# Optimization experiments

Measured on AMD Instinct MI355X. Metric: run time of the kernel, lower is better.

Reference implementation:

```python
import jax, jax.numpy as jnp
import numpy as np
from jax import lax

DN = ('NCHW', 'OIHW', 'NCHW')

def conv7(x, w, b):
    y = lax.conv_general_dilated(x, w, window_strides=(1, 1), padding='VALID', dimension_numbers=DN)
    return y + b[None, :, None, None]

def maxpool2(x):
    return lax.reduce_window(x, -jnp.inf, lax.max, (1, 1, 2, 2), (1, 1, 2, 2), 'VALID')

def setup_inputs() -> dict:
    key = jax.random.key(0)
    ks = jax.random.split(key, 7)
    B, C, H, W = 8, 64, 70, 70
    x = jax.random.normal(ks[0], (B, C, H, W), dtype=jnp.float32)
    s = 0.05  # small init to keep softmax logits sane
    theta_w = jax.random.normal(ks[1], (100, C, 7, 7), dtype=jnp.float32) * s
    theta_b = jax.random.normal(ks[2], (100,), dtype=jnp.float32) * s
    phi_w = jax.random.normal(ks[3], (100, C, 7, 7), dtype=jnp.float32) * s
    phi_b = jax.random.normal(ks[4], (100,), dtype=jnp.float32) * s
    g_w = jax.random.normal(ks[5], (200, C, 7, 7), dtype=jnp.float32) * s
    g_b = jax.random.normal(ks[6], (200,), dtype=jnp.float32) * s
    return {'x': x, 'theta_w': theta_w, 'theta_b': theta_b, 'phi_w': phi_w, 'phi_b': phi_b, 'g_w': g_w, 'g_b': g_b}

def reference(x, theta_w, theta_b, phi_w, phi_b, g_w, g_b):
    B, C, H, W = x.shape
    h, w = H - 6, W - 6           # VALID 7x7 conv output spatial
    N = h * w                     # 4096
    M = N // 4                    # 1024 (after 2x2 maxpool)
    theta = conv7(x, theta_w, theta_b).reshape(B, 100, N)
    phi = maxpool2(conv7(x, phi_w, phi_b)).reshape(B, 100, M)
    attn = jnp.einsum('bcn,bcm->bnm', theta, phi)                # B x N x M
    attn = jax.nn.softmax(attn, axis=-1)
    g = maxpool2(conv7(x, g_w, g_b)).reshape(B, 200, M)
    attn_g = jnp.einsum('bcm,bnm->bcn', g, attn)
    return attn_g.reshape(B, 200, h, w)
```

## Files before the change

### kernel.cpp

```cpp
#include <hip/hip_runtime.h>
#include <cstdint>
#include <cstddef>

#define BATCH 8
#define CIN 64
#define HIN 70
#define HOUT 64
#define NPIX 4096
#define MPIX 1024

typedef __attribute__((ext_vector_type(8))) short short8;
typedef __attribute__((ext_vector_type(4))) float f32x4;
typedef __attribute__((ext_vector_type(4))) unsigned int uint4v;

__device__ __forceinline__ unsigned short f2bf_rne(float f) {
  unsigned int u = __builtin_bit_cast(unsigned int, f);
  unsigned int r = (u + 0x7FFFu + ((u >> 16) & 1u)) >> 16;
  return (unsigned short)r;
}

__device__ __forceinline__ unsigned int rot16(unsigned int u) {
  return (u >> 16) | (u << 16);
}

__global__ __launch_bounds__(256) void prep_x(const float* __restrict__ x,
                                              unsigned int* __restrict__ xTi) {
  __shared__ float tile[64][71];
  const int blk = blockIdx.x;
  const int b = blk / 70;
  const int r = blk - b * 70;
  const int t = threadIdx.x;
  for (int i = t; i < 64 * 70; i += 256) {
    int ci = i / 70;
    int c = i - ci * 70;
    tile[ci][c] = x[(((size_t)(b * 64 + ci)) * 70 + r) * 70 + c];
  }
  __syncthreads();
  for (int i = t; i < 70 * 64; i += 256) {
    int c = i >> 6;
    int ci = i & 63;
    float a = tile[ci][c];
    unsigned short hi = f2bf_rne(a);
    float hif = __builtin_bit_cast(float, ((unsigned int)hi) << 16);
    unsigned short lo = f2bf_rne(a - hif);
    xTi[(((size_t)(b * 70 + r)) * 70 + c) * 64 + ci] =
        (unsigned int)hi | (((unsigned int)lo) << 16);
  }
}

__global__ __launch_bounds__(256) void prep_w(
    const float* __restrict__ tw, const float* __restrict__ pw,
    const float* __restrict__ gw,
    const float* __restrict__ tb, const float* __restrict__ pb,
    const float* __restrict__ gb,
    unsigned int* __restrict__ wTi, float* __restrict__ biasPad) {
  int gid = blockIdx.x * 256 + threadIdx.x;
  if (gid >= 49 * 448 * 64) return;
  if (gid < 448) {
    float bv = 0.0f;
    if (gid < 100) bv = tb[gid];
    else if (gid < 200) bv = pb[gid - 100];
    else if (gid < 400) bv = gb[gid - 200];
    biasPad[gid] = bv;
  }
  int ci = gid & 63;
  int OC = (gid >> 6) % 448;
  int s = gid / (448 * 64);
  float v = 0.0f;
  if (OC < 100) v = tw[((size_t)(OC * 64 + ci)) * 49 + s];
  else if (OC < 200) v = pw[((size_t)((OC - 100) * 64 + ci)) * 49 + s];
  else if (OC < 400) v = gw[((size_t)((OC - 200) * 64 + ci)) * 49 + s];
  unsigned short hi = f2bf_rne(v);
  float hif = __builtin_bit_cast(float, ((unsigned int)hi) << 16);
  unsigned short lo = f2bf_rne(v - hif);
  wTi[gid] = (unsigned int)hi | (((unsigned int)lo) << 16);
}

__global__ __launch_bounds__(512, 2) void convmfma_kernel(
    const unsigned short* __restrict__ xTi,
    const unsigned short* __restrict__ wTi,
    const float* __restrict__ biasPad,
    unsigned int* __restrict__ thd_dw,
    unsigned int* __restrict__ phd_dw,
    unsigned short* __restrict__ gP) {
  __shared__ __align__(16) char smem[62720 + 16384];
  const int LDSW = 62720;

  const int gx = blockIdx.x;
  const int b = gx >> 3;
  const int ptile = gx & 7;
  const int oy0 = ptile * 8;
  const int oc0 = blockIdx.y << 6;

  const int t = threadIdx.x;
  const int wv = t >> 6;
  const int l = t & 63;
  const int lm = l & 15;
  const int lg = l >> 4;
  const int py = oy0 + wv;

  const int sub = t >> 8;
  const int oc_t = (t >> 2) & 63;
  const int q = t & 3;
  const int wdstOff =
      sub * 4096 + (oc_t << 6) + ((q << 4) ^ (((oc_t >> 1) & 3) << 4));
  const int keyA = ((lm >> 1) & 3) << 4;
  const int laneA = (lm << 6) + ((lg << 4) ^ keyA);

  f32x4 acc[4][4];
#pragma unroll
  for (int j = 0; j < 4; ++j)
#pragma unroll
    for (int f = 0; f < 4; ++f) acc[j][f] = (f32x4)0.0f;

  for (int chunk = 0; chunk < 4; ++chunk) {
    for (int i = t; i < 3920; i += 512) {
      int idx70 = i >> 2;
      int s16 = i & 3;
      int rr = idx70 / 70;
      int cc = idx70 - rr * 70;
      const unsigned short* src =
          xTi + ((((size_t)(b * 70 + oy0 + rr)) * 70 + cc) << 7) +
          (chunk << 5) + (s16 << 3);
      short8 v = *(const short8*)src;
      int dst = (idx70 << 6) + ((s16 << 4) ^ (((cc >> 1) & 3) << 4));
      *(short8*)(smem + dst) = v;
    }
    const unsigned short* wsrcBase =
        wTi + ((size_t)(oc0 + oc_t) << 7) + (chunk << 5) + (q << 3);
    short8 wreg = *(const short8*)(wsrcBase + (size_t)sub * 57344);
    *(short8*)(smem + LDSW + wdstOff) = wreg;
    wreg = *(const short8*)(wsrcBase + (size_t)(2 + sub) * 57344);
    __syncthreads();

    for (int p = 0; p < 25; ++p) {
      const char* slotBase = smem + LDSW + ((p & 1) << 13);
#pragma unroll
      for (int halfs = 0; halfs < 2; ++halfs) {
        const int s = 2 * p + halfs;
        if (s <= 48) {
          const int ky = s / 7;
          const int kx = s - ky * 7;
          const char* wb = slotBase + (halfs << 12) + laneA;
          short8 aW[4], aS[4];
#pragma unroll
          for (int j = 0; j < 4; ++j) {
            aW[j] = *(const short8*)(wb + j * 1024);
            uint4v u = __builtin_bit_cast(uint4v, aW[j]);
            u.x = rot16(u.x); u.y = rot16(u.y);
            u.z = rot16(u.z); u.w = rot16(u.w);
            aS[j] = __builtin_bit_cast(short8, u);
          }
          const int klx = kx + lm;
          const int key = ((klx >> 1) & 3) << 4;
          const char* bbase =
              smem + ((wv + ky) * 70 + klx) * 64 + ((lg << 4) ^ key);
#pragma unroll
          for (int f = 0; f < 4; ++f) {
            short8 bf = *(const short8*)(bbase + f * 1024);
#pragma unroll
            for (int j = 0; j < 4; ++j) {
              acc[j][f] = __builtin_amdgcn_mfma_f32_16x16x32_bf16(
                  aW[j], bf, acc[j][f], 0, 0, 0);
              acc[j][f] = __builtin_amdgcn_mfma_f32_16x16x32_bf16(
                  aS[j], bf, acc[j][f], 0, 0, 0);
            }
          }
        }
      }
      if (p < 24) {
        *(short8*)(smem + LDSW + (((p + 1) & 1) << 13) + wdstOff) = wreg;
        if (p < 23) {
          int snext = 2 * (p + 2) + sub;
          if (snext > 48) snext = 48;
          wreg = *(const short8*)(wsrcBase + (size_t)snext * 57344);
        }
      }
      __syncthreads();
    }
  }

  float bia[4][4];
#pragma unroll
  for (int j = 0; j < 4; ++j)
#pragma unroll
    for (int r = 0; r < 4; ++r) bia[j][r] = biasPad[oc0 + j * 16 + lg * 4 + r];

#pragma unroll
  for (int j = 0; j < 4; ++j) {
#pragma unroll
    for (int f = 0; f < 4; ++f) {
#pragma unroll
      for (int r = 0; r < 4; ++r) {
        int ch = oc0 + j * 16 + lg * 4 + r;
        int n = py * 64 + f * 16 + lm;
        if (ch < 100) {
          float v = acc[j][f][r] + bia[j][r];
          unsigned short hi = f2bf_rne(v);
          float hif = __builtin_bit_cast(float, ((unsigned int)hi) << 16);
          unsigned short lo = f2bf_rne(v - hif);
          thd_dw[(((size_t)(b << 12) + n) << 7) + ch] =
              (unsigned int)hi | (((unsigned int)lo) << 16);
        } else if (ch < 128) {
          thd_dw[(((size_t)(b << 12) + n) << 7) + ch] = 0u;
        }
      }
    }
  }

  __syncthreads();
  float* scratch = (float*)smem;

#pragma unroll
  for (int j = 0; j < 4; ++j) {
#pragma unroll
    for (int f = 0; f < 4; ++f) {
#pragma unroll
      for (int r = 0; r < 4; ++r) {
        float v = acc[j][f][r] + bia[j][r];
        float vn = fmaxf(v, __shfl_xor(v, 1));
        acc[j][f][r] = vn;
        if ((wv & 1) && !(lm & 1)) {
          int ch_local = j * 16 + lg * 4 + r;
          int mcol = f * 8 + (lm >> 1);
          scratch[(wv >> 1) * 2112 + ch_local * 33 + mcol] = vn;
        }
      }
    }
  }
  __syncthreads();

  if (!(wv & 1)) {
#pragma unroll
    for (int j = 0; j < 4; ++j) {
#pragma unroll
      for (int f = 0; f < 4; ++f) {
#pragma unroll
        for (int r = 0; r < 4; ++r) {
          if (!(lm & 1)) {
            int ch = oc0 + j * 16 + lg * 4 + r;
            int ch_local = j * 16 + lg * 4 + r;
            int mcol = f * 8 + (lm >> 1);
            float partner = scratch[(wv >> 1) * 2112 + ch_local * 33 + mcol];
            float vfinal = fmaxf(acc[j][f][r], partner);
            int m = (((oy0 >> 1) + (wv >> 1)) << 5) + mcol;
            if (ch >= 100 && ch < 200) {
              int c = ch - 100;
              unsigned short hi = f2bf_rne(vfinal);
              float hif = __builtin_bit_cast(float, ((unsigned int)hi) << 16);
              unsigned short lo = f2bf_rne(vfinal - hif);
              phd_dw[(((size_t)(b << 10) + m) << 7) + c] =
                  (unsigned int)hi | (((unsigned int)lo) << 16);
            } else if (ch >= 200 && ch < 408) {
              int cg = ch - 200;
              gP[((size_t)(b * 208 + cg) << 10) + m] = f2bf_rne(vfinal);
              if (ch < 228) {
                phd_dw[(((size_t)(b << 10) + m) << 7) + (ch - 100)] = 0u;
              }
            }
          }
        }
      }
    }
  }
}

__global__ __launch_bounds__(256) void attn_kernel(
    const unsigned short* __restrict__ thd,
    const unsigned short* __restrict__ phd,
    const unsigned short* __restrict__ gP,
    float* __restrict__ out) {
  __shared__ __align__(16) float outAcc[16][212];
  __shared__ float corrL[16][33];
  __shared__ float statsL[4][16][2];
  __shared__ float mFinL[16];
  __shared__ float invL[16];

  const int bx = blockIdx.x;
  const int b = bx >> 8;
  const int n0 = (bx & 255) << 4;
  const int t = threadIdx.x;
  const int w = t >> 6;
  const int l = t & 63;
  const int lm = l & 15;
  const int lg = l >> 4;

  short8 aA[8], aS[8];
  {
    const unsigned short* ap =
        thd + (((size_t)(b << 12) + n0 + lm) << 8) + lg * 8;
#pragma unroll
    for (int kf = 0; kf < 8; ++kf) {
      short8 v = *(const short8*)(ap + kf * 32);
      aA[kf] = v;
      uint4v u = __builtin_bit_cast(uint4v, v);
      u.x = rot16(u.x); u.y = rot16(u.y); u.z = rot16(u.z); u.w = rot16(u.w);
      aS[kf] = __builtin_bit_cast(short8, u);
    }
  }

  float mRun = -3.0e38f, sRun = 0.0f;
  unsigned int Pr[8][4];

  const int src1 = ((lg & 1) << 5) + lm;
  const int src2 = src1 + 16;
  const bool hi2 = (lg >> 1) != 0;

#pragma unroll
  for (int step = 0; step < 8; ++step) {
    const int m0 = (w << 8) + (step << 5);
    f32x4 ac0 = (f32x4)0.f, ac1 = (f32x4)0.f;
    const unsigned short* bp0 =
        phd + (((size_t)(b << 10) + m0 + lm) << 8) + lg * 8;
    const unsigned short* bp1 = bp0 + (16 << 8);
#pragma unroll
    for (int kf = 0; kf < 8; ++kf) {
      short8 av0 = *(const short8*)(bp0 + kf * 32);
      short8 av1 = *(const short8*)(bp1 + kf * 32);
      ac0 = __builtin_amdgcn_mfma_f32_16x16x32_bf16(av0, aA[kf], ac0, 0, 0, 0);
      ac1 = __builtin_amdgcn_mfma_f32_16x16x32_bf16(av1, aA[kf], ac1, 0, 0, 0);
      ac0 = __builtin_amdgcn_mfma_f32_16x16x32_bf16(av0, aS[kf], ac0, 0, 0, 0);
      ac1 = __builtin_amdgcn_mfma_f32_16x16x32_bf16(av1, aS[kf], ac1, 0, 0, 0);
    }
    float tm = fmaxf(fmaxf(fmaxf(ac0[0], ac0[1]), fmaxf(ac0[2], ac0[3])),
                     fmaxf(fmaxf(ac1[0], ac1[1]), fmaxf(ac1[2], ac1[3])));
    tm = fmaxf(tm, __shfl_xor(tm, 16));
    tm = fmaxf(tm, __shfl_xor(tm, 32));
    float mNew = fmaxf(mRun, tm);
    float scale = __expf(mRun - mNew);
    float p0 = __expf(ac0[0] - mNew), p1 = __expf(ac0[1] - mNew);
    float p2 = __expf(ac0[2] - mNew), p3 = __expf(ac0[3] - mNew);
    float q0 = __expf(ac1[0] - mNew), q1 = __expf(ac1[1] - mNew);
    float q2 = __expf(ac1[2] - mNew), q3 = __expf(ac1[3] - mNew);
    float cs = ((p0 + p1) + (p2 + p3)) + ((q0 + q1) + (q2 + q3));
    cs += __shfl_xor(cs, 16);
    cs += __shfl_xor(cs, 32);
    mRun = mNew;
    sRun = sRun * scale + cs;
    if (l < 16) corrL[lm][(w << 3) + step] = mRun;
    unsigned int d0 = (unsigned int)f2bf_rne(p0) |
                      (((unsigned int)f2bf_rne(p1)) << 16);
    unsigned int d1 = (unsigned int)f2bf_rne(p2) |
                      (((unsigned int)f2bf_rne(p3)) << 16);
    unsigned int e0 = (unsigned int)f2bf_rne(q0) |
                      (((unsigned int)f2bf_rne(q1)) << 16);
    unsigned int e1 = (unsigned int)f2bf_rne(q2) |
                      (((unsigned int)f2bf_rne(q3)) << 16);
    unsigned int A0 = (unsigned int)__shfl((int)d0, src1);
    unsigned int A1 = (unsigned int)__shfl((int)d1, src1);
    unsigned int B0 = (unsigned int)__shfl((int)d0, src2);
    unsigned int B1 = (unsigned int)__shfl((int)d1, src2);
    unsigned int C0 = (unsigned int)__shfl((int)e0, src1);
    unsigned int C1 = (unsigned int)__shfl((int)e1, src1);
    unsigned int D0 = (unsigned int)__shfl((int)e0, src2);
    unsigned int D1 = (unsigned int)__shfl((int)e1, src2);
    Pr[step][0] = hi2 ? C0 : A0;
    Pr[step][1] = hi2 ? C1 : A1;
    Pr[step][2] = hi2 ? D0 : B0;
    Pr[step][3] = hi2 ? D1 : B1;
  }
  if (l < 16) {
    statsL[w][lm][0] = mRun;
    statsL[w][lm][1] = sRun;
  }
  __syncthreads();

  if (t < 16) {
    float mF = -3.0e38f;
#pragma unroll
    for (int qq = 0; qq < 4; ++qq) mF = fmaxf(mF, statsL[qq][t][0]);
    float sF = 0.0f;
#pragma unroll
    for (int qq = 0; qq < 4; ++qq)
      sF += statsL[qq][t][1] * __expf(statsL[qq][t][0] - mF);
    mFinL[t] = mF;
    invL[t] = 1.0f / sF;
  }
  __syncthreads();

  {
    int e = t * 2;
#pragma unroll
    for (int i = 0; i < 2; ++i) {
      int row = (e + i) >> 5;
      int col = (e + i) & 31;
      corrL[row][col] = __expf(corrL[row][col] - mFinL[row]) * invL[row];
    }
  }
  __syncthreads();

#pragma unroll
  for (int s = 0; s < 8; ++s) {
    float corr = corrL[lm][(w << 3) + s];
#pragma unroll
    for (int j = 0; j < 4; ++j) {
      unsigned int u = Pr[s][j];
      float lo = __builtin_bit_cast(float, u << 16);
      float hi = __builtin_bit_cast(float, u & 0xffff0000u);
      Pr[s][j] = (unsigned int)f2bf_rne(lo * corr) |
                 (((unsigned int)f2bf_rne(hi * corr)) << 16);
    }
  }

  f32x4 oacc[13];
#pragma unroll
  for (int i = 0; i < 13; ++i) oacc[i] = (f32x4)0.f;

#pragma unroll
  for (int s = 0; s < 8; ++s) {
    uint4v pu;
    pu.x = Pr[s][0]; pu.y = Pr[s][1]; pu.z = Pr[s][2]; pu.w = Pr[s][3];
    short8 pf = __builtin_bit_cast(short8, pu);
    const unsigned short* gbase =
        gP + ((size_t)(b * 208) << 10) + (w << 8) + (s << 5) + lg * 8;
#pragma unroll
    for (int ct = 0; ct < 13; ++ct) {
      int c = (ct << 4) + lm;
      short8 gv = *(const short8*)(gbase + ((size_t)c << 10));
      oacc[ct] = __builtin_amdgcn_mfma_f32_16x16x32_bf16(pf, gv, oacc[ct], 0, 0, 0);
    }
  }

  for (int rnd = 0; rnd < 4; ++rnd) {
    if (w == rnd) {
#pragma unroll
      for (int ct = 0; ct < 13; ++ct) {
#pragma unroll
        for (int r = 0; r < 4; ++r) {
          int n = (lg << 2) + r;
          int c = (ct << 4) + lm;
          if (rnd == 0) outAcc[n][c] = oacc[ct][r];
          else outAcc[n][c] += oacc[ct][r];
        }
      }
    }
    __syncthreads();
  }

  {
    int lane16 = t & 15;
    int grp = t >> 4;
    for (int c = grp; c < 200; c += 16)
      out[(((size_t)(b * 200 + c)) << 12) + n0 + lane16] = outAcc[lane16][c];
  }
}

extern "C" void kernel_launch(void* const* d_in, const int* in_sizes, int n_in,
                              void* d_out, int out_size, void* d_ws,
                              size_t ws_size, hipStream_t stream) {
  const float* x  = (const float*)d_in[0];
  const float* tw = (const float*)d_in[1];
  const float* tb = (const float*)d_in[2];
  const float* pw = (const float*)d_in[3];
  const float* pb = (const float*)d_in[4];
  const float* gw = (const float*)d_in[5];
  const float* gb = (const float*)d_in[6];
  float* out = (float*)d_out;

  unsigned short* ws_us = (unsigned short*)d_ws;
  unsigned short* thd = ws_us;
  unsigned short* phd = ws_us + 8388608;
  unsigned short* gP  = ws_us + 10485760;
  unsigned short* xTi = ws_us + 12189696;
  unsigned short* wTi = ws_us + 17207296;
  float* biasPad = (float*)(ws_us + 20017152);

  prep_x<<<560, 256, 0, stream>>>(x, (unsigned int*)xTi);
  prep_w<<<5488, 256, 0, stream>>>(tw, pw, gw, tb, pb, gb,
                                   (unsigned int*)wTi, biasPad);

  convmfma_kernel<<<dim3(64, 7), 512, 0, stream>>>(
      xTi, wTi, biasPad, (unsigned int*)thd, (unsigned int*)phd, gP);
  attn_kernel<<<2048, 256, 0, stream>>>(thd, phd, gP, out);
}
```

Before: 502.6 us.

## Split conv into dual-bf16 theta/phi pass and single-bf16 g pass

The conv kernel is split into two template instantiations. Channels 0-255 (theta, phi and part of g) keep the hi/lo split-bf16 path with two MFMAs per product. Channels 256-447, which are only g outputs, use plain bf16 inputs with a single MFMA and half the input channels to stage, so less matrix work is spent on g. Blocks now use 256 threads, each wave computing two output rows, which lets the 2x2 maxpool happen mostly in registers instead of through LDS scratch. The price is reduced precision on part of g, extra prep buffers, and an extra launch.

Result: faster. 445.1 us (-11.4%).

```diff
diff --git a/kernel.cpp b/kernel.cpp
--- a/kernel.cpp
+++ b/kernel.cpp
@@ -24,7 +24,8 @@
 }
 
 __global__ __launch_bounds__(256) void prep_x(const float* __restrict__ x,
-                                              unsigned int* __restrict__ xTi) {
+                                              unsigned int* __restrict__ xTi,
+                                              unsigned int* __restrict__ xTi_h) {
   __shared__ float tile[64][71];
   const int blk = blockIdx.x;
   const int b = blk / 70;
@@ -46,6 +47,13 @@
     xTi[(((size_t)(b * 70 + r)) * 70 + c) * 64 + ci] =
         (unsigned int)hi | (((unsigned int)lo) << 16);
   }
+  for (int i = t; i < 70 * 32; i += 256) {
+    int c = i >> 5;
+    int dwi = i & 31;
+    unsigned int h0 = f2bf_rne(tile[2 * dwi][c]);
+    unsigned int h1 = f2bf_rne(tile[2 * dwi + 1][c]);
+    xTi_h[(((size_t)(b * 70 + r)) * 70 + c) * 32 + dwi] = h0 | (h1 << 16);
+  }
 }
 
 __global__ __launch_bounds__(256) void prep_w(
@@ -53,84 +61,112 @@
     const float* __restrict__ gw,
     const float* __restrict__ tb, const float* __restrict__ pb,
     const float* __restrict__ gb,
-    unsigned int* __restrict__ wTi, float* __restrict__ biasPad) {
+    unsigned int* __restrict__ wTi, unsigned int* __restrict__ wTi_s,
+    float* __restrict__ biasPad) {
   int gid = blockIdx.x * 256 + threadIdx.x;
-  if (gid >= 49 * 448 * 64) return;
-  if (gid < 448) {
-    float bv = 0.0f;
-    if (gid < 100) bv = tb[gid];
-    else if (gid < 200) bv = pb[gid - 100];
-    else if (gid < 400) bv = gb[gid - 200];
-    biasPad[gid] = bv;
-  }
-  int ci = gid & 63;
-  int OC = (gid >> 6) % 448;
-  int s = gid / (448 * 64);
-  float v = 0.0f;
-  if (OC < 100) v = tw[((size_t)(OC * 64 + ci)) * 49 + s];
-  else if (OC < 200) v = pw[((size_t)((OC - 100) * 64 + ci)) * 49 + s];
-  else if (OC < 400) v = gw[((size_t)((OC - 200) * 64 + ci)) * 49 + s];
-  unsigned short hi = f2bf_rne(v);
-  float hif = __builtin_bit_cast(float, ((unsigned int)hi) << 16);
-  unsigned short lo = f2bf_rne(v - hif);
-  wTi[gid] = (unsigned int)hi | (((unsigned int)lo) << 16);
-}
-
-__global__ __launch_bounds__(512, 2) void convmfma_kernel(
-    const unsigned short* __restrict__ xTi,
-    const unsigned short* __restrict__ wTi,
+  if (gid < 1404928) {
+    if (gid < 448) {
+      float bv = 0.0f;
+      if (gid < 100) bv = tb[gid];
+      else if (gid < 200) bv = pb[gid - 100];
+      else if (gid < 400) bv = gb[gid - 200];
+      biasPad[gid] = bv;
+    }
+    int ci = gid & 63;
+    int OC = (gid >> 6) % 448;
+    int s = gid / (448 * 64);
+    float v = 0.0f;
+    if (OC < 100) v = tw[((size_t)(OC * 64 + ci)) * 49 + s];
+    else if (OC < 200) v = pw[((size_t)((OC - 100) * 64 + ci)) * 49 + s];
+    else if (OC < 400) v = gw[((size_t)((OC - 200) * 64 + ci)) * 49 + s];
+    unsigned short hi = f2bf_rne(v);
+    float hif = __builtin_bit_cast(float, ((unsigned int)hi) << 16);
+    unsigned short lo = f2bf_rne(v - hif);
+    wTi[gid] = (unsigned int)hi | (((unsigned int)lo) << 16);
+  } else if (gid < 1404928 + 301056) {
+    int g2 = gid - 1404928;
+    int dwi = g2 & 31;
+    int OCl = (g2 >> 5) % 192;
+    int s = g2 / (192 * 32);
+    int gc = 56 + OCl;
+    float v0 = 0.0f, v1 = 0.0f;
+    if (gc < 200) {
+      v0 = gw[((size_t)(gc * 64 + 2 * dwi)) * 49 + s];
+      v1 = gw[((size_t)(gc * 64 + 2 * dwi + 1)) * 49 + s];
+    }
+    wTi_s[g2] = (unsigned int)f2bf_rne(v0) |
+                (((unsigned int)f2bf_rne(v1)) << 16);
+  }
+}
+
+template <bool DUAL>
+__global__ __launch_bounds__(256, 2) void convmfma_kernel(
+    const unsigned short* __restrict__ xT,
+    const unsigned short* __restrict__ wT,
     const float* __restrict__ biasPad,
     unsigned int* __restrict__ thd_dw,
     unsigned int* __restrict__ phd_dw,
     unsigned short* __restrict__ gP) {
   __shared__ __align__(16) char smem[62720 + 16384];
   const int LDSW = 62720;
+  const int NCH = DUAL ? 4 : 2;
+  const int XS = DUAL ? 128 : 64;
+  const int WOCS = DUAL ? 128 : 64;
+  const int WSTRIDE = DUAL ? 57344 : 12288;
 
   const int gx = blockIdx.x;
   const int b = gx >> 3;
   const int ptile = gx & 7;
   const int oy0 = ptile * 8;
-  const int oc0 = blockIdx.y << 6;
+  const int oc0 = (DUAL ? 0 : 256) + (blockIdx.y << 6);
+  const int oc0W = DUAL ? oc0 : (blockIdx.y << 6);
 
   const int t = threadIdx.x;
   const int wv = t >> 6;
   const int l = t & 63;
   const int lm = l & 15;
   const int lg = l >> 4;
-  const int py = oy0 + wv;
-
-  const int sub = t >> 8;
-  const int oc_t = (t >> 2) & 63;
-  const int q = t & 3;
-  const int wdstOff =
-      sub * 4096 + (oc_t << 6) + ((q << 4) ^ (((oc_t >> 1) & 3) << 4));
+
+  int wdstOff_[2];
+  const unsigned short* wsrc_[2];
   const int keyA = ((lm >> 1) & 3) << 4;
   const int laneA = (lm << 6) + ((lg << 4) ^ keyA);
 
-  f32x4 acc[4][4];
+  f32x4 acc[4][2][4];
 #pragma unroll
   for (int j = 0; j < 4; ++j)
 #pragma unroll
-    for (int f = 0; f < 4; ++f) acc[j][f] = (f32x4)0.0f;
-
-  for (int chunk = 0; chunk < 4; ++chunk) {
-    for (int i = t; i < 3920; i += 512) {
+    for (int rr = 0; rr < 2; ++rr)
+#pragma unroll
+      for (int f = 0; f < 4; ++f) acc[j][rr][f] = (f32x4)0.0f;
+
+  for (int chunk = 0; chunk < NCH; ++chunk) {
+    for (int i = t; i < 3920; i += 256) {
       int idx70 = i >> 2;
       int s16 = i & 3;
       int rr = idx70 / 70;
       int cc = idx70 - rr * 70;
       const unsigned short* src =
-          xTi + ((((size_t)(b * 70 + oy0 + rr)) * 70 + cc) << 7) +
+          xT + ((size_t)((b * 70 + oy0 + rr) * 70 + cc)) * XS +
           (chunk << 5) + (s16 << 3);
       short8 v = *(const short8*)src;
       int dst = (idx70 << 6) + ((s16 << 4) ^ (((cc >> 1) & 3) << 4));
       *(short8*)(smem + dst) = v;
     }
-    const unsigned short* wsrcBase =
-        wTi + ((size_t)(oc0 + oc_t) << 7) + (chunk << 5) + (q << 3);
-    short8 wreg = *(const short8*)(wsrcBase + (size_t)sub * 57344);
-    *(short8*)(smem + LDSW + wdstOff) = wreg;
-    wreg = *(const short8*)(wsrcBase + (size_t)(2 + sub) * 57344);
+    short8 wreg[2];
+#pragma unroll
+    for (int u2 = 0; u2 < 2; ++u2) {
+      int u = t + (u2 << 8);
+      int sub = u >> 8;
+      int oc_t = (u >> 2) & 63;
+      int q = u & 3;
+      wdstOff_[u2] =
+          sub * 4096 + (oc_t << 6) + ((q << 4) ^ (((oc_t >> 1) & 3) << 4));
+      wsrc_[u2] = wT + (size_t)(oc0W + oc_t) * WOCS + (chunk << 5) + (q << 3);
+      wreg[u2] = *(const short8*)(wsrc_[u2] + (size_t)sub * WSTRIDE);
+      *(short8*)(smem + LDSW + wdstOff_[u2]) = wreg[u2];
+      wreg[u2] = *(const short8*)(wsrc_[u2] + (size_t)(2 + sub) * WSTRIDE);
+    }
     __syncthreads();
 
     for (int p = 0; p < 25; ++p) {
@@ -146,34 +182,45 @@
 #pragma unroll
           for (int j = 0; j < 4; ++j) {
             aW[j] = *(const short8*)(wb + j * 1024);
-            uint4v u = __builtin_bit_cast(uint4v, aW[j]);
-            u.x = rot16(u.x); u.y = rot16(u.y);
-            u.z = rot16(u.z); u.w = rot16(u.w);
-            aS[j] = __builtin_bit_cast(short8, u);
+            if (DUAL) {
+              uint4v u = __builtin_bit_cast(uint4v, aW[j]);
+              u.x = rot16(u.x); u.y = rot16(u.y);
+              u.z = rot16(u.z); u.w = rot16(u.w);
+              aS[j] = __builtin_bit_cast(short8, u);
+            }
           }
           const int klx = kx + lm;
           const int key = ((klx >> 1) & 3) << 4;
-          const char* bbase =
-              smem + ((wv + ky) * 70 + klx) * 64 + ((lg << 4) ^ key);
-#pragma unroll
-          for (int f = 0; f < 4; ++f) {
-            short8 bf = *(const short8*)(bbase + f * 1024);
-#pragma unroll
-            for (int j = 0; j < 4; ++j) {
-              acc[j][f] = __builtin_amdgcn_mfma_f32_16x16x32_bf16(
-                  aW[j], bf, acc[j][f], 0, 0, 0);
-              acc[j][f] = __builtin_amdgcn_mfma_f32_16x16x32_bf16(
-                  aS[j], bf, acc[j][f], 0, 0, 0);
+#pragma unroll
+          for (int rr = 0; rr < 2; ++rr) {
+            const char* bbase =
+                smem + ((2 * wv + rr + ky) * 70 + klx) * 64 + ((lg << 4) ^ key);
+#pragma unroll
+            for (int f = 0; f < 4; ++f) {
+              short8 bf = *(const short8*)(bbase + f * 1024);
+#pragma unroll
+              for (int j = 0; j < 4; ++j) {
+                acc[j][rr][f] = __builtin_amdgcn_mfma_f32_16x16x32_bf16(
+                    aW[j], bf, acc[j][rr][f], 0, 0, 0);
+                if (DUAL)
+                  acc[j][rr][f] = __builtin_amdgcn_mfma_f32_16x16x32_bf16(
+                      aS[j], bf, acc[j][rr][f], 0, 0, 0);
+              }
             }
           }
         }
       }
       if (p < 24) {
-        *(short8*)(smem + LDSW + (((p + 1) & 1) << 13) + wdstOff) = wreg;
-        if (p < 23) {
-          int snext = 2 * (p + 2) + sub;
-          if (snext > 48) snext = 48;
-          wreg = *(const short8*)(wsrcBase + (size_t)snext * 57344);
+#pragma unroll
+        for (int u2 = 0; u2 < 2; ++u2) {
+          *(short8*)(smem + LDSW + (((p + 1) & 1) << 13) + wdstOff_[u2]) =
+              wreg[u2];
+          if (p < 23) {
+            int sub = (t + (u2 << 8)) >> 8;
+            int snext = 2 * (p + 2) + sub;
+            if (snext > 48) snext = 48;
+            wreg[u2] = *(const short8*)(wsrc_[u2] + (size_t)snext * WSTRIDE);
+          }
         }
       }
       __syncthreads();
@@ -186,78 +233,65 @@
 #pragma unroll
     for (int r = 0; r < 4; ++r) bia[j][r] = biasPad[oc0 + j * 16 + lg * 4 + r];
 
-#pragma unroll
-  for (int j = 0; j < 4; ++j) {
-#pragma unroll
-    for (int f = 0; f < 4; ++f) {
-#pragma unroll
-      for (int r = 0; r < 4; ++r) {
-        int ch = oc0 + j * 16 + lg * 4 + r;
-        int n = py * 64 + f * 16 + lm;
-        if (ch < 100) {
-          float v = acc[j][f][r] + bia[j][r];
-          unsigned short hi = f2bf_rne(v);
-          float hif = __builtin_bit_cast(float, ((unsigned int)hi) << 16);
-          unsigned short lo = f2bf_rne(v - hif);
-          thd_dw[(((size_t)(b << 12) + n) << 7) + ch] =
-              (unsigned int)hi | (((unsigned int)lo) << 16);
-        } else if (ch < 128) {
-          thd_dw[(((size_t)(b << 12) + n) << 7) + ch] = 0u;
+  if (DUAL) {
+#pragma unroll
+    for (int j = 0; j < 4; ++j) {
+#pragma unroll
+      for (int rr = 0; rr < 2; ++rr) {
+#pragma unroll
+        for (int f = 0; f < 4; ++f) {
+#pragma unroll
+          for (int r = 0; r < 4; ++r) {
+            int ch = oc0 + j * 16 + lg * 4 + r;
+            if (ch < 128) {
+              int n = (oy0 + 2 * wv + rr) * 64 + f * 16 + lm;
+              unsigned int outw = 0u;
+              if (ch < 100) {
+                float v = acc[j][rr][f][r] + bia[j][r];
+                unsigned short hi = f2bf_rne(v);
+                float hif =
+                    __builtin_bit_cast(float, ((unsigned int)hi) << 16);
+                unsigned short lo = f2bf_rne(v - hif);
+                outw = (unsigned int)hi | (((unsigned int)lo) << 16);
+              }
+              thd_dw[(((size_t)(b << 12) + n) << 7) + ch] = outw;
+            }
+          }
         }
       }
     }
   }
 
-  __syncthreads();
-  float* scratch = (float*)smem;
-
 #pragma unroll
   for (int j = 0; j < 4; ++j) {
 #pragma unroll
     for (int f = 0; f < 4; ++f) {
 #pragma unroll
       for (int r = 0; r < 4; ++r) {
-        float v = acc[j][f][r] + bia[j][r];
-        float vn = fmaxf(v, __shfl_xor(v, 1));
-        acc[j][f][r] = vn;
-        if ((wv & 1) && !(lm & 1)) {
-          int ch_local = j * 16 + lg * 4 + r;
-          int mcol = f * 8 + (lm >> 1);
-          scratch[(wv >> 1) * 2112 + ch_local * 33 + mcol] = vn;
-        }
-      }
-    }
-  }
-  __syncthreads();
-
-  if (!(wv & 1)) {
-#pragma unroll
-    for (int j = 0; j < 4; ++j) {
-#pragma unroll
-      for (int f = 0; f < 4; ++f) {
-#pragma unroll
-        for (int r = 0; r < 4; ++r) {
-          if (!(lm & 1)) {
-            int ch = oc0 + j * 16 + lg * 4 + r;
-            int ch_local = j * 16 + lg * 4 + r;
-            int mcol = f * 8 + (lm >> 1);
-            float partner = scratch[(wv >> 1) * 2112 + ch_local * 33 + mcol];
-            float vfinal = fmaxf(acc[j][f][r], partner);
-            int m = (((oy0 >> 1) + (wv >> 1)) << 5) + mcol;
+        float v0 = acc[j][0][f][r] + bia[j][r];
+        float v1 = acc[j][1][f][r] + bia[j][r];
+        float vr = fmaxf(v0, v1);
+        float vn = fmaxf(vr, __shfl_xor(vr, 1));
+        if (!(lm & 1)) {
+          int ch = oc0 + j * 16 + lg * 4 + r;
+          int m = (((oy0 >> 1) + wv) << 5) + f * 8 + (lm >> 1);
+          if (DUAL) {
             if (ch >= 100 && ch < 200) {
               int c = ch - 100;
-              unsigned short hi = f2bf_rne(vfinal);
+              unsigned short hi = f2bf_rne(vn);
               float hif = __builtin_bit_cast(float, ((unsigned int)hi) << 16);
-              unsigned short lo = f2bf_rne(vfinal - hif);
+              unsigned short lo = f2bf_rne(vn - hif);
               phd_dw[(((size_t)(b << 10) + m) << 7) + c] =
                   (unsigned int)hi | (((unsigned int)lo) << 16);
-            } else if (ch >= 200 && ch < 408) {
-              int cg = ch - 200;
-              gP[((size_t)(b * 208 + cg) << 10) + m] = f2bf_rne(vfinal);
-              if (ch < 228) {
+            } else if (ch >= 200) {
+              gP[((size_t)(b * 208 + (ch - 200)) << 10) + m] = f2bf_rne(vn);
+              if (ch < 228)
                 phd_dw[(((size_t)(b << 10) + m) << 7) + (ch - 100)] = 0u;
-              }
             }
+          } else {
+            int cg = ch - 200;
+            if (cg < 208)
+              gP[((size_t)(b * 208 + cg) << 10) + m] = f2bf_rne(vn);
           }
         }
       }
@@ -458,18 +492,23 @@
   float* out = (float*)d_out;
 
   unsigned short* ws_us = (unsigned short*)d_ws;
-  unsigned short* thd = ws_us;
-  unsigned short* phd = ws_us + 8388608;
-  unsigned short* gP  = ws_us + 10485760;
-  unsigned short* xTi = ws_us + 12189696;
-  unsigned short* wTi = ws_us + 17207296;
-  float* biasPad = (float*)(ws_us + 20017152);
-
-  prep_x<<<560, 256, 0, stream>>>(x, (unsigned int*)xTi);
-  prep_w<<<5488, 256, 0, stream>>>(tw, pw, gw, tb, pb, gb,
-                                   (unsigned int*)wTi, biasPad);
-
-  convmfma_kernel<<<dim3(64, 7), 512, 0, stream>>>(
+  unsigned short* thd   = ws_us;
+  unsigned short* phd   = ws_us + 8388608;
+  unsigned short* gP    = ws_us + 10485760;
+  unsigned short* xTi   = ws_us + 12189696;
+  unsigned short* wTi   = ws_us + 17207296;
+  unsigned short* xTi_h = ws_us + 20017152;
+  unsigned short* wTi_s = ws_us + 22525952;
+  float* biasPad = (float*)(ws_us + 23128064);
+
+  prep_x<<<560, 256, 0, stream>>>(x, (unsigned int*)xTi, (unsigned int*)xTi_h);
+  prep_w<<<6664, 256, 0, stream>>>(tw, pw, gw, tb, pb, gb,
+                                   (unsigned int*)wTi, (unsigned int*)wTi_s,
+                                   biasPad);
+
+  convmfma_kernel<true><<<dim3(64, 4), 256, 0, stream>>>(
       xTi, wTi, biasPad, (unsigned int*)thd, (unsigned int*)phd, gP);
+  convmfma_kernel<false><<<dim3(64, 3), 256, 0, stream>>>(
+      xTi_h, wTi_s, biasPad, (unsigned int*)thd, (unsigned int*)phd, gP);
   attn_kernel<<<2048, 256, 0, stream>>>(thd, phd, gP, out);
 }
```
